# Optimization experiments

Measured on AMD Instinct MI355X. Metric: run time of the kernel, lower is better.

## Reference

```python
import jax, jax.numpy as jnp
import numpy as np

U, I, D = 100000, 200000, 64   # users, items, emb_size
N = U + I                      # total nodes
NNZ = 6400000                  # adjacency non-zeros
B = 4096                       # batch of (user,item) pairs
L = 3                          # n_layers


def setup_inputs() -> dict:
    key = jax.random.key(0)
    ks = jax.random.split(key, 11)
    s = 1.0 / np.sqrt(D)  # xavier-ish scale
    return {
        "user_emb_online": jax.random.normal(ks[0], (U, D), jnp.float32) * s,
        "item_emb_online": jax.random.normal(ks[1], (I, D), jnp.float32) * s,
        "user_emb_target": jax.random.normal(ks[2], (U, D), jnp.float32) * s,
        "item_emb_target": jax.random.normal(ks[3], (I, D), jnp.float32) * s,
        # normalized adjacency values (positive, roughly 1/deg scale)
        "adj_val": jax.random.uniform(ks[4], (NNZ,), jnp.float32) * (1.0 / 16.0),
        "pred_w": jax.random.normal(ks[5], (D, D), jnp.float32) * s,
        "pred_b": jnp.zeros((D,), jnp.float32),
        "adj_row": jax.random.randint(ks[6], (NNZ,), 0, N, dtype=jnp.int32),
        "adj_col": jax.random.randint(ks[7], (NNZ,), 0, N, dtype=jnp.int32),
        "user_idx": jax.random.randint(ks[8], (B,), 0, U, dtype=jnp.int32),
        "item_idx": jax.random.randint(ks[9], (B,), 0, I, dtype=jnp.int32),
    }


def _spmm(row, col, val, x):
    # sparse [N,N] @ dense [N,D] via gather + segment-sum
    return jax.ops.segment_sum(val[:, None] * x[col], row, num_segments=N)


def _lgcn_encode(user_emb, item_emb, row, col, val):
    ego = jnp.concatenate([user_emb, item_emb], axis=0)  # [N, D]
    acc = ego
    x = ego
    for _ in range(L):
        x = _spmm(row, col, val, x)
        acc = acc + x
    all_emb = acc / (L + 1)  # mean over stacked layer outputs
    return all_emb[:U], all_emb[U:]


def reference(user_emb_online, item_emb_online, user_emb_target, item_emb_target,
              adj_val, pred_w, pred_b, adj_row, adj_col, user_idx, item_idx):
    u_on_all, i_on_all = _lgcn_encode(user_emb_online, item_emb_online, adj_row, adj_col, adj_val)
    u_tg_all, i_tg_all = _lgcn_encode(user_emb_target, item_emb_target, adj_row, adj_col, adj_val)
    u_online = u_on_all[user_idx]   # [B, D]
    i_online = i_on_all[item_idx]
    u_target = u_tg_all[user_idx]
    i_target = i_tg_all[item_idx]
    u_pred = u_online @ pred_w.T + pred_b  # nn.Linear
    i_pred = i_online @ pred_w.T + pred_b
    return (u_pred, u_target, i_pred, i_target)
```

## Files before the change

kernel.cpp:

```cpp
#include <hip/hip_runtime.h>
#include <hip/hip_bf16.h>
#include <stdint.h>

#define U_N   100000
#define I_N   200000
#define NN    300000
#define DD    64
#define NNZ_N 6400000
#define BB    4096
#define CHUNK 4096
#define NB    ((NN + CHUNK - 1) / CHUNK)
#define NBK   74
#define EPB   4096
#define NSB   1184
#define SUBCAP 6656
#define BKCAP  94208
#define BKBLK  23
#define LBLK   48000

typedef unsigned short u16;
typedef unsigned int   u32;
typedef float vf2 __attribute__((ext_vector_type(2)));

__device__ __forceinline__ u16 f2bf(float f) {
    u32 u = __float_as_uint(f);
    u32 r = (u + 0x7FFFu + ((u >> 16) & 1u)) >> 16;
    return (u16)r;
}


#if __has_builtin(__builtin_amdgcn_cvt_pk_f32_fp8) && __has_builtin(__builtin_amdgcn_cvt_pk_fp8_f32)
#define FP8_HW 1
#else
#define FP8_HW 0
#endif

__device__ __forceinline__ u32 enc1_fp8(float f) {
    float af = fabsf(f);
    u32 s = (__float_as_uint(f) >> 31) << 7;
    if (af >= 0.015625f) {
        u32 au = __float_as_uint(af);
        u32 r = au + 0x7FFFFu + ((au >> 20) & 1u);
        u32 e = (r >> 23) - 120u;
        u32 m = (r >> 20) & 7u;
        if (e > 15u) { e = 15u; m = 6u; }
        return s | (e << 3) | m;
    } else {
        u32 q = (u32)__float2int_rn(af * 512.0f);
        return s | q;
    }
}

__device__ __forceinline__ u32 pack4_fp8(float a, float b, float c, float d) {
#if FP8_HW
    u32 w = 0;
    w = (u32)__builtin_amdgcn_cvt_pk_fp8_f32(a, b, (int)w, false);
    w = (u32)__builtin_amdgcn_cvt_pk_fp8_f32(c, d, (int)w, true);
    return w;
#else
    return enc1_fp8(a) | (enc1_fp8(b) << 8) | (enc1_fp8(c) << 16) | (enc1_fp8(d) << 24);
#endif
}

__device__ __forceinline__ float dec1_fp8(u32 b) {
    u32 s = (b & 0x80u) << 24;
    u32 e = (b >> 3) & 15u;
    u32 m = b & 7u;
    float mag = e ? __uint_as_float(((e + 120u) << 23) | (m << 20))
                  : (float)m * 0.001953125f;
    return __uint_as_float(__float_as_uint(mag) | s);
}

__device__ __forceinline__ void dec_fp8x4(u32 w, float* f) {
#if FP8_HW
    vf2 lo = __builtin_amdgcn_cvt_pk_f32_fp8((int)w, false);
    vf2 hi = __builtin_amdgcn_cvt_pk_f32_fp8((int)w, true);
    f[0] = lo[0]; f[1] = lo[1]; f[2] = hi[0]; f[3] = hi[1];
#else
    f[0] = dec1_fp8(w & 255u); f[1] = dec1_fp8((w >> 8) & 255u);
    f[2] = dec1_fp8((w >> 16) & 255u); f[3] = dec1_fp8(w >> 24);
#endif
}


__global__ void setup_k(unsigned char* __restrict__ mark, unsigned char* __restrict__ bmark,
                        int* __restrict__ nlist, int* __restrict__ bkt_cursor) {
    int tid = blockIdx.x * 256 + threadIdx.x;
    if (tid < NN / 4) { ((u32*)mark)[tid] = 0; ((u32*)bmark)[tid] = 0; }
    if (tid < NBK) bkt_cursor[tid] = tid * BKCAP;
    if (tid == NN / 4) nlist[0] = 0;
}


__global__ __launch_bounds__(256) void p1_k(const int* __restrict__ adj_row,
                                            const int* __restrict__ adj_col,
                                            const float* __restrict__ adj_val,
                                            int* __restrict__ bkt_cursor,
                                            u32* __restrict__ bpk,
                                            float* __restrict__ bval) {
    __shared__ int lcnt[NBK];
    __shared__ int lbase[NBK];
    int base = blockIdx.x * EPB;
    for (int i = threadIdx.x; i < NBK; i += 256) lcnt[i] = 0;
    __syncthreads();
    u32 pk[16]; float vv[16]; int bb[16]; int rk[16];
#pragma unroll
    for (int j = 0; j < 16; j++) {
        int e = base + j * 256 + threadIdx.x;
        bb[j] = -1;
        if (e < NNZ_N) {
            int r = adj_row[e];
            int c = adj_col[e];
            vv[j] = adj_val[e];
            int b = r >> 12;
            pk[j] = ((u32)(r & 4095) << 19) | (u32)c;
            bb[j] = b;
            rk[j] = atomicAdd(&lcnt[b], 1);
        }
    }
    __syncthreads();
    for (int i = threadIdx.x; i < NBK; i += 256)
        lbase[i] = atomicAdd(&bkt_cursor[i], lcnt[i]);
    __syncthreads();
#pragma unroll
    for (int j = 0; j < 16; j++) {
        if (bb[j] >= 0) {
            int p = lbase[bb[j]] + rk[j];
            bpk[p]  = pk[j];
            bval[p] = vv[j];
        }
    }
}


__global__ __launch_bounds__(1024) void bhist_k(const int* __restrict__ bkt_cursor,
                                                const u32* __restrict__ bpk,
                                                int* __restrict__ cnt) {
    __shared__ int h[4096];
    int b = blockIdx.x;
    int base = b * BKCAP;
    int e1 = bkt_cursor[b];
    for (int j = threadIdx.x; j < 4096; j += 1024) h[j] = 0;
    __syncthreads();
    for (int i = base + threadIdx.x; i < e1; i += 1024)
        atomicAdd(&h[bpk[i] >> 19], 1);
    __syncthreads();
    int rb = b << 12;
    for (int j = threadIdx.x; j < 4096; j += 1024) {
        int idx = rb + j;
        if (idx < NN) cnt[idx] = h[j];
    }
}


__global__ void scan1_k(const int* __restrict__ cnt, int* __restrict__ bsums) {
    __shared__ int red[256];
    int base = blockIdx.x * CHUNK;
    int s = 0;
    for (int j = threadIdx.x; j < CHUNK; j += 256) {
        int idx = base + j;
        s += (idx < NN) ? cnt[idx] : 0;
    }
    red[threadIdx.x] = s;
    __syncthreads();
    for (int o = 128; o > 0; o >>= 1) {
        if (threadIdx.x < o) red[threadIdx.x] += red[threadIdx.x + o];
        __syncthreads();
    }
    if (threadIdx.x == 0) bsums[blockIdx.x] = red[0];
}

__global__ void scan2_k(int* __restrict__ bsums, int* __restrict__ row_ptr) {
    __shared__ int sh[128];
    int v = (threadIdx.x < NB) ? bsums[threadIdx.x] : 0;
    sh[threadIdx.x] = v;
    __syncthreads();
    for (int o = 1; o < 128; o <<= 1) {
        int t = (threadIdx.x >= o) ? sh[threadIdx.x - o] : 0;
        __syncthreads();
        sh[threadIdx.x] += t;
        __syncthreads();
    }
    if (threadIdx.x < NB) bsums[threadIdx.x] = sh[threadIdx.x] - v;
    if (threadIdx.x == 127) row_ptr[NN] = sh[127];
}

__global__ void scan3_k(const int* __restrict__ cnt, const int* __restrict__ bsums,
                        int* __restrict__ row_ptr, int* __restrict__ sub_cursor) {
    __shared__ int tsum[256];
    int base = blockIdx.x * CHUNK;
    int loc[16];
    int s = 0;
#pragma unroll
    for (int j = 0; j < 16; j++) {
        int idx = base + threadIdx.x * 16 + j;
        int c = (idx < NN) ? cnt[idx] : 0;
        loc[j] = s;
        s += c;
    }
    tsum[threadIdx.x] = s;
    __syncthreads();
    int v = s;
    for (int o = 1; o < 256; o <<= 1) {
        int t = (threadIdx.x >= o) ? tsum[threadIdx.x - o] : 0;
        __syncthreads();
        tsum[threadIdx.x] += t;
        __syncthreads();
    }
    int texcl = tsum[threadIdx.x] - v;
    int boff = bsums[blockIdx.x];
#pragma unroll
    for (int j = 0; j < 16; j++) {
        int idx = base + threadIdx.x * 16 + j;
        if (idx < NN) {
            int val = boff + texcl + loc[j];
            row_ptr[idx] = val;
            if ((idx & 255) == 0) sub_cursor[idx >> 8] = val;
        }
    }
}


__global__ __launch_bounds__(256) void p2r_k(const int* __restrict__ bkt_cursor,
                                             const u32* __restrict__ bpk,
                                             const float* __restrict__ bval,
                                             int* __restrict__ sub_cursor,
                                             int2* __restrict__ mid) {
    __shared__ int lcnt[16], lbase[16], sbase[16];
    __shared__ int2 stage[4096];
    int b = blockIdx.y;
    int e1 = bkt_cursor[b];
    int base = b * BKCAP + blockIdx.x * 4096;
    if (base >= e1) return;
    if (threadIdx.x < 16) lcnt[threadIdx.x] = 0;
    __syncthreads();
    u32 pk[16]; float vv[16]; int sb[16], rk[16];
#pragma unroll
    for (int j = 0; j < 16; j++) {
        int e = base + j * 256 + threadIdx.x;
        sb[j] = -1;
        if (e < e1) {
            pk[j] = bpk[e];
            vv[j] = bval[e];
            int s = (int)((pk[j] >> 27) & 15u);
            sb[j] = s;
            rk[j] = atomicAdd(&lcnt[s], 1);
        }
    }
    __syncthreads();
    if (threadIdx.x == 0) {
        int acc = 0;
#pragma unroll
        for (int s = 0; s < 16; s++) { sbase[s] = acc; acc += lcnt[s]; }
    }
    if (threadIdx.x < 16)
        lbase[threadIdx.x] = atomicAdd(&sub_cursor[b * 16 + threadIdx.x], lcnt[threadIdx.x]);
    __syncthreads();
#pragma unroll
    for (int j = 0; j < 16; j++)
        if (sb[j] >= 0)
            stage[sbase[sb[j]] + rk[j]] = make_int2((int)pk[j], __float_as_int(vv[j]));
    __syncthreads();
    for (int s = 0; s < 16; s++) {
        int c = lcnt[s], gb = lbase[s], lb = sbase[s];
        for (int i = threadIdx.x; i < c; i += 256)
            mid[gb + i] = stage[lb + i];
    }
}


__global__ __launch_bounds__(256) void p3_k(const int* __restrict__ row_ptr,
                                            const int2* __restrict__ mid,
                                            int2* __restrict__ edge_s) {
    __shared__ int rbase[256], rcur[256];
    __shared__ int2 stage[SUBCAP];
    int s = blockIdx.x;
    int r0 = s << 8;
    if (r0 >= NN) return;
    int r1 = min(r0 + 256, NN);
    int nr = r1 - r0;
    int ebase = row_ptr[r0];
    int eend  = row_ptr[r1];
    int cnt = eend - ebase;
    if (threadIdx.x < nr) {
        rbase[threadIdx.x] = row_ptr[r0 + threadIdx.x] - ebase;
        rcur[threadIdx.x] = 0;
    }
    __syncthreads();
    for (int i = threadIdx.x; i < cnt; i += 256) {
        int2 d = mid[ebase + i];
        u32 pk = (u32)d.x;
        int l = (int)((pk >> 19) & 255u);
        int pos = rbase[l] + atomicAdd(&rcur[l], 1);
        if (pos < SUBCAP) stage[pos] = make_int2((int)(pk & 0x7FFFFu), d.y);
    }
    __syncthreads();
    for (int i = threadIdx.x; i < cnt; i += 256) edge_s[ebase + i] = stage[i];
}


__global__ void mark_k(const int* __restrict__ row_ptr, const int2* __restrict__ edge_s,
                       const int* __restrict__ user_idx, const int* __restrict__ item_idx,
                       unsigned char* __restrict__ mark, unsigned char* __restrict__ bmark) {
    int wave = threadIdx.x >> 6;
    int lane = threadIdx.x & 63;
    int slot = blockIdx.x * 4 + wave;
    if (slot >= 2 * BB) return;
    int r = (slot < BB) ? user_idx[slot] : U_N + item_idx[slot - BB];
    if (lane == 0) { mark[r] = 1; bmark[r] = 1; }
    int e0 = row_ptr[r], e1 = row_ptr[r + 1];
    for (int e = e0 + lane; e < e1; e += 64) mark[edge_s[e].x] = 1;
}

__global__ void compact_k(const unsigned char* __restrict__ mark,
                          int* __restrict__ list2, int* __restrict__ nlist) {
    int i = blockIdx.x * 256 + threadIdx.x;
    int lane = threadIdx.x & 63;
    int m = (i < NN) ? (int)mark[i] : 0;
    unsigned long long b = __ballot(m != 0);
    int pre = __popcll(b & ((1ull << lane) - 1ull));
    int tot = __popcll(b);
    int base = 0;
    if (lane == 0 && tot) base = atomicAdd(nlist, tot);
    base = __shfl(base, 0);
    if (m) list2[base + pre] = i;
}


__global__ void pack1_k(const float* __restrict__ ue_on, const float* __restrict__ ie_on,
                        const float* __restrict__ ue_tg, const float* __restrict__ ie_tg,
                        unsigned char* __restrict__ x0f) {
    int tid = blockIdx.x * blockDim.x + threadIdx.x;
    int n = tid >> 4;
    int t = tid & 15;
    if (n >= NN) return;
    const float* src;
    int soff;
    if (t < 8) {
        soff = t * 8;
        src = (n < U_N) ? ue_on + (size_t)n * 64 : ie_on + (size_t)(n - U_N) * 64;
    } else {
        soff = (t - 8) * 8;
        src = (n < U_N) ? ue_tg + (size_t)n * 64 : ie_tg + (size_t)(n - U_N) * 64;
    }
    float4 f0 = *(const float4*)(src + soff);
    float4 f1 = *(const float4*)(src + soff + 4);
    uint2 o;
    o.x = pack4_fp8(f0.x, f0.y, f0.z, f0.w);
    o.y = pack4_fp8(f1.x, f1.y, f1.z, f1.w);
    *(uint2*)(x0f + (size_t)n * 128 + t * 8) = o;
}


struct acc8 { float a[8]; };

__device__ __forceinline__ void red8(acc8& A) {
#pragma unroll
    for (int k = 0; k < 8; k++) {
        A.a[k] += __shfl_xor(A.a[k], 16);
        A.a[k] += __shfl_xor(A.a[k], 32);
    }
}

__device__ __forceinline__ void rg8_core(const int2* __restrict__ edge_s,
                                         const unsigned char* __restrict__ xf,
                                         int t, int g, int e0, int e1, acc8& A) {
#pragma unroll
    for (int k = 0; k < 8; k++) A.a[k] = 0.f;
    const unsigned char* xt = xf + t * 8;
    int d = e1 - e0;

    int2 ed[8];
    uint2 pv[8];
#pragma unroll
    for (int q = 0; q < 8; q++) { ed[q] = make_int2(0, 0); pv[q] = make_uint2(0u, 0u); }
#pragma unroll
    for (int q = 0; q < 8; q++) {
        int j = g + 4 * q;
        if (j < d) ed[q] = edge_s[e0 + j];
    }
#pragma unroll
    for (int q = 0; q < 8; q++) {
        int j = g + 4 * q;
        if (j < d) pv[q] = *(const uint2*)(xt + (size_t)((u32)ed[q].x * 128u));
    }
#pragma unroll
    for (int q = 0; q < 8; q++) {
        float v = __int_as_float(ed[q].y);
        float f[8];
        dec_fp8x4(pv[q].x, f);
        dec_fp8x4(pv[q].y, f + 4);
#pragma unroll
        for (int k = 0; k < 8; k++) A.a[k] += v * f[k];
    }
    for (int e = e0 + 32 + g * 4; e < e1; e += 16) {
        int m = e1 - e;
#pragma unroll
        for (int k = 0; k < 4; k++) {
            if (k < m) {
                int2 dd = edge_s[e + k];
                float v = __int_as_float(dd.y);
                uint2 p = *(const uint2*)(xt + (size_t)((u32)dd.x * 128u));
                float f[8];
                dec_fp8x4(p.x, f);
                dec_fp8x4(p.y, f + 4);
#pragma unroll
                for (int q = 0; q < 8; q++) A.a[q] += v * f[q];
            }
        }
    }
    red8(A);
}

__global__ __launch_bounds__(256) void spmm1_k(const int* __restrict__ row_ptr,
                                               const int2* __restrict__ edge_s,
                                               const unsigned char* __restrict__ x0f,
                                               const unsigned char* __restrict__ bmark,
                                               u16* __restrict__ y,
                                               unsigned char* __restrict__ yf) {
    int lane = threadIdx.x & 63;
    int t = lane & 15, g = lane >> 4;
    int r = blockIdx.x * 4 + (threadIdx.x >> 6);
    if (r >= NN) return;
    acc8 A;
    rg8_core(edge_s, x0f, t, g, row_ptr[r], row_ptr[r + 1], A);
    if (g == 0) {
        uint2 of;
        of.x = pack4_fp8(A.a[0], A.a[1], A.a[2], A.a[3]);
        of.y = pack4_fp8(A.a[4], A.a[5], A.a[6], A.a[7]);
        *(uint2*)(yf + (size_t)r * 128 + t * 8) = of;
        if (bmark[r]) {
            uint4 o;
            o.x = ((u32)f2bf(A.a[1]) << 16) | (u32)f2bf(A.a[0]);
            o.y = ((u32)f2bf(A.a[3]) << 16) | (u32)f2bf(A.a[2]);
            o.z = ((u32)f2bf(A.a[5]) << 16) | (u32)f2bf(A.a[4]);
            o.w = ((u32)f2bf(A.a[7]) << 16) | (u32)f2bf(A.a[6]);
            *(uint4*)(y + (size_t)r * 128 + t * 8) = o;
        }
    }
}

__device__ __forceinline__ void rg16_core(const int2* __restrict__ edge_s,
                                          const u16* __restrict__ x,
                                          int t, int g, int e0, int e1, acc8& A) {
#pragma unroll
    for (int k = 0; k < 8; k++) A.a[k] = 0.f;
    const u16* xt = x + t * 8;
    int d = e1 - e0;

    int2 ed[8];
    uint4 pv[8];
#pragma unroll
    for (int q = 0; q < 8; q++) { ed[q] = make_int2(0, 0); pv[q] = make_uint4(0u, 0u, 0u, 0u); }
#pragma unroll
    for (int q = 0; q < 8; q++) {
        int j = g + 4 * q;
        if (j < d) ed[q] = edge_s[e0 + j];
    }
#pragma unroll
    for (int q = 0; q < 8; q++) {
        int j = g + 4 * q;
        if (j < d) pv[q] = *(const uint4*)(xt + (size_t)(u32)ed[q].x * 128);
    }
#pragma unroll
    for (int q = 0; q < 8; q++) {
        float v = __int_as_float(ed[q].y);
        A.a[0] += v * __uint_as_float(pv[q].x << 16);
        A.a[1] += v * __uint_as_float(pv[q].x & 0xFFFF0000u);
        A.a[2] += v * __uint_as_float(pv[q].y << 16);
        A.a[3] += v * __uint_as_float(pv[q].y & 0xFFFF0000u);
        A.a[4] += v * __uint_as_float(pv[q].z << 16);
        A.a[5] += v * __uint_as_float(pv[q].z & 0xFFFF0000u);
        A.a[6] += v * __uint_as_float(pv[q].w << 16);
        A.a[7] += v * __uint_as_float(pv[q].w & 0xFFFF0000u);
    }
    for (int e = e0 + 32 + g * 4; e < e1; e += 16) {
        int m = e1 - e;
#pragma unroll
        for (int k = 0; k < 4; k++) {
            if (k < m) {
                int2 dd = edge_s[e + k];
                float v = __int_as_float(dd.y);
                uint4 p = *(const uint4*)(xt + (size_t)(u32)dd.x * 128);
                A.a[0] += v * __uint_as_float(p.x << 16);
                A.a[1] += v * __uint_as_float(p.x & 0xFFFF0000u);
                A.a[2] += v * __uint_as_float(p.y << 16);
                A.a[3] += v * __uint_as_float(p.y & 0xFFFF0000u);
                A.a[4] += v * __uint_as_float(p.z << 16);
                A.a[5] += v * __uint_as_float(p.z & 0xFFFF0000u);
                A.a[6] += v * __uint_as_float(p.w << 16);
                A.a[7] += v * __uint_as_float(p.w & 0xFFFF0000u);
            }
        }
    }
    red8(A);
}

__global__ __launch_bounds__(256) void spmm_list_k(const int* __restrict__ row_ptr,
                                                   const int2* __restrict__ edge_s,
                                                   const unsigned char* __restrict__ x1f,
                                                   u16* __restrict__ y,
                                                   const int* __restrict__ list2,
                                                   const int* __restrict__ nlist) {
    int lane = threadIdx.x & 63;
    int t = lane & 15, g = lane >> 4;
    int slot = blockIdx.x * 4 + (threadIdx.x >> 6);
    if (slot >= *nlist) return;
    int r = list2[slot];
    acc8 A;
    rg8_core(edge_s, x1f, t, g, row_ptr[r], row_ptr[r + 1], A);
    if (g == 0) {
        uint4 o;
        o.x = ((u32)f2bf(A.a[1]) << 16) | (u32)f2bf(A.a[0]);
        o.y = ((u32)f2bf(A.a[3]) << 16) | (u32)f2bf(A.a[2]);
        o.z = ((u32)f2bf(A.a[5]) << 16) | (u32)f2bf(A.a[4]);
        o.w = ((u32)f2bf(A.a[7]) << 16) | (u32)f2bf(A.a[6]);
        *(uint4*)(y + (size_t)r * 128 + t * 8) = o;
    }
}

__global__ __launch_bounds__(256) void spmm_last_k(const int* __restrict__ row_ptr,
                                                   const int2* __restrict__ edge_s,
                                                   const u16* __restrict__ x,
                                                   const int* __restrict__ user_idx,
                                                   const int* __restrict__ item_idx,
                                                   float* __restrict__ out_acc) {
    int lane = threadIdx.x & 63;
    int t = lane & 15, g = lane >> 4;
    int slot = blockIdx.x * 4 + (threadIdx.x >> 6);
    if (slot >= 2 * BB) return;
    int r = (slot < BB) ? user_idx[slot] : U_N + item_idx[slot - BB];
    acc8 A;
    rg16_core(edge_s, x, t, g, row_ptr[r], row_ptr[r + 1], A);
    if (g == 0) {
        uint4 p = *(const uint4*)(x + (size_t)r * 128 + t * 8);
        A.a[0] += __uint_as_float(p.x << 16);
        A.a[1] += __uint_as_float(p.x & 0xFFFF0000u);
        A.a[2] += __uint_as_float(p.y << 16);
        A.a[3] += __uint_as_float(p.y & 0xFFFF0000u);
        A.a[4] += __uint_as_float(p.z << 16);
        A.a[5] += __uint_as_float(p.z & 0xFFFF0000u);
        A.a[6] += __uint_as_float(p.w << 16);
        A.a[7] += __uint_as_float(p.w & 0xFFFF0000u);
        float4* p0 = (float4*)(out_acc + (size_t)slot * 128 + t * 8);
        float4 c0 = p0[0], c1 = p0[1];
        c0.x += A.a[0]; c0.y += A.a[1]; c0.z += A.a[2]; c0.w += A.a[3];
        c1.x += A.a[4]; c1.y += A.a[5]; c1.z += A.a[6]; c1.w += A.a[7];
        p0[0] = c0; p0[1] = c1;
    }
}


__global__ void init_acc_k(const int* __restrict__ user_idx, const int* __restrict__ item_idx,
                           const float* __restrict__ ue_on, const float* __restrict__ ie_on,
                           const float* __restrict__ ue_tg, const float* __restrict__ ie_tg,
                           float* __restrict__ out_acc) {
    int t = blockIdx.x * blockDim.x + threadIdx.x;
    int slot = t >> 5;
    int j = t & 31;
    if (slot >= 2 * BB) return;
    int node = (slot < BB) ? user_idx[slot] : U_N + item_idx[slot - BB];
    const float* src;
    int soff, doff;
    if (j < 16) {
        soff = j * 4; doff = j * 4;
        src = (node < U_N) ? ue_on + (size_t)node * 64 : ie_on + (size_t)(node - U_N) * 64;
    } else {
        soff = (j - 16) * 4; doff = 64 + (j - 16) * 4;
        src = (node < U_N) ? ue_tg + (size_t)node * 64 : ie_tg + (size_t)(node - U_N) * 64;
    }
    float4 f = *(const float4*)(src + soff);
    *(float4*)(out_acc + (size_t)slot * 128 + doff) = f;
}

__global__ void gadd_k(const int* __restrict__ user_idx, const int* __restrict__ item_idx,
                       const u16* __restrict__ x, float* __restrict__ out_acc) {
    int t = blockIdx.x * blockDim.x + threadIdx.x;
    int slot = t >> 6;
    int l = t & 63;
    if (slot >= 2 * BB) return;
    int node = (slot < BB) ? user_idx[slot] : U_N + item_idx[slot - BB];
    u32 p = *(const u32*)(x + (size_t)node * 128 + (l << 1));
    float fx = __uint_as_float(p << 16);
    float fy = __uint_as_float(p & 0xFFFF0000u);
    float2* q = (float2*)(out_acc + (size_t)slot * 128) + l;
    float2 cur = *q;
    cur.x += fx; cur.y += fy;
    *q = cur;
}


__global__ __launch_bounds__(256) void pred_k(const float* __restrict__ out_acc,
                                              const float* __restrict__ W,
                                              const float* __restrict__ bias,
                                              float* __restrict__ out) {
    __shared__ float wld[64 * 65];
    __shared__ float uld[4 * 64];
    int j = threadIdx.x & 63;
    int rl = threadIdx.x >> 6;
    for (int i = threadIdx.x; i < 4096; i += 256) {
        int jj = i >> 6, kk = i & 63;
        wld[kk * 65 + jj] = W[i];
    }
    int slot = blockIdx.x * 4 + rl;
    uld[rl * 64 + j] = out_acc[(size_t)slot * 128 + j] * 0.25f;
    float tv = out_acc[(size_t)slot * 128 + 64 + j] * 0.25f;
    size_t tdst = (slot < BB) ? (size_t)BB * 64 + (size_t)slot * 64 + j
                              : (size_t)3 * BB * 64 + (size_t)(slot - BB) * 64 + j;
    out[tdst] = tv;
    __syncthreads();
    float acc = bias[j];
#pragma unroll
    for (int k = 0; k < 64; k++) acc += uld[rl * 64 + k] * wld[k * 65 + j];
    size_t dst = (slot < BB) ? (size_t)slot * 64 + j
                             : (size_t)2 * BB * 64 + (size_t)(slot - BB) * 64 + j;
    out[dst] = acc;
}


extern "C" void kernel_launch(void* const* d_in, const int* in_sizes, int n_in,
                              void* d_out, int out_size, void* d_ws, size_t ws_size,
                              hipStream_t stream) {
    const float* ue_on = (const float*)d_in[0];
    const float* ie_on = (const float*)d_in[1];
    const float* ue_tg = (const float*)d_in[2];
    const float* ie_tg = (const float*)d_in[3];
    const float* adj_val = (const float*)d_in[4];
    const float* pred_w = (const float*)d_in[5];
    const float* pred_b = (const float*)d_in[6];
    const int* adj_row = (const int*)d_in[7];
    const int* adj_col = (const int*)d_in[8];
    const int* user_idx = (const int*)d_in[9];
    const int* item_idx = (const int*)d_in[10];
    float* out = (float*)d_out;

    char* ws = (char*)d_ws;
    size_t off = 0;
    auto alloc = [&](size_t bytes) -> char* {
        char* p = ws + off;
        off = (off + bytes + 255) & ~(size_t)255;
        return p;
    };
    int*   cnt        = (int*)alloc((size_t)NN * 4);
    int*   row_ptr    = (int*)alloc((size_t)(NN + 1) * 4);
    int*   bsums      = (int*)alloc(256 * 4);
    int*   bkt_cursor = (int*)alloc(256 * 4);
    int*   sub_cursor = (int*)alloc((size_t)NSB * 4);
    unsigned char* mark = (unsigned char*)alloc((size_t)NN);
    unsigned char* bmark = (unsigned char*)alloc((size_t)NN);
    int*   list2      = (int*)alloc((size_t)NN * 4);
    int*   nlist      = (int*)alloc(256 * 4);
    int2*  edge_s     = (int2*)alloc((size_t)NNZ_N * 8);
    u16*   x_a        = (u16*)alloc((size_t)NN * 128 * 2);
    u16*   x_b        = (u16*)alloc((size_t)NN * 128 * 2);
    float* out_acc    = (float*)alloc((size_t)2 * BB * 128 * 4);

    u32*   bpk  = (u32*)x_a;
    unsigned char* x0f = (unsigned char*)x_a;
    unsigned char* x1f = (unsigned char*)x_a + (size_t)NN * 128;
    float* bval = (float*)x_b;
    int2*  mid  = edge_s;

    (void)n_in; (void)in_sizes; (void)out_size; (void)ws_size;

    setup_k<<<294, 256, 0, stream>>>(mark, bmark, nlist, bkt_cursor);
    p1_k<<<(NNZ_N + EPB - 1) / EPB, 256, 0, stream>>>(adj_row, adj_col, adj_val, bkt_cursor, bpk, bval);
    bhist_k<<<NBK, 1024, 0, stream>>>(bkt_cursor, bpk, cnt);
    scan1_k<<<NB, 256, 0, stream>>>(cnt, bsums);
    scan2_k<<<1, 128, 0, stream>>>(bsums, row_ptr);
    scan3_k<<<NB, 256, 0, stream>>>(cnt, bsums, row_ptr, sub_cursor);
    p2r_k<<<dim3(BKBLK, NBK), 256, 0, stream>>>(bkt_cursor, bpk, bval, sub_cursor, mid);
    p3_k<<<NSB, 256, 0, stream>>>(row_ptr, mid, edge_s);

    mark_k<<<(2 * BB) / 4, 256, 0, stream>>>(row_ptr, edge_s, user_idx, item_idx, mark, bmark);
    compact_k<<<(NN + 255) / 256, 256, 0, stream>>>(mark, list2, nlist);

    pack1_k<<<(NN * 16 + 255) / 256, 256, 0, stream>>>(ue_on, ie_on, ue_tg, ie_tg, x0f);
    init_acc_k<<<(2 * BB * 32) / 256, 256, 0, stream>>>(user_idx, item_idx, ue_on, ie_on, ue_tg, ie_tg, out_acc);

    spmm1_k<<<NN / 4, 256, 0, stream>>>(row_ptr, edge_s, x0f, bmark, x_b, x1f);
    gadd_k<<<(2 * BB * 64) / 256, 256, 0, stream>>>(user_idx, item_idx, x_b, out_acc);
    spmm_list_k<<<LBLK, 256, 0, stream>>>(row_ptr, edge_s, x1f, x_b, list2, nlist);
    spmm_last_k<<<(2 * BB) / 4, 256, 0, stream>>>(row_ptr, edge_s, x_b, user_idx, item_idx, out_acc);

    pred_k<<<(2 * BB) / 4, 256, 0, stream>>>(out_acc, pred_w, pred_b, out);
}
```

Before: 748.0 us.

## Fuse bucketing, fp8 packing and acc init; derive scan sums from bucket counts

Merges the edge bucketing pass, the fp8 packing of input embeddings and the batch accumulator init into one launch using block-index ranges. It also folds the bucket histogram and the block-sum scan into a single kernel, taking per-chunk sums straight from bucket cursors, since bucket size equals chunk size. The bucketed keys move to the upper half of x_b so packing into x_a does not clash. This cuts launch overhead and lets independent work overlap, at the cost of more register pressure in the combined kernels.

```diff
diff --git a/kernel.cpp b/kernel.cpp
--- a/kernel.cpp
+++ b/kernel.cpp
@@ -17,6 +17,9 @@
 #define BKCAP  94208
 #define BKBLK  23
 #define LBLK   48000
+#define P1B   ((NNZ_N + EPB - 1) / EPB)
+#define PACKB ((NN * 16) / 256)
+#define ACCB  ((2 * BB * 32) / 256)
 
 typedef unsigned short u16;
 typedef unsigned int   u32;
@@ -92,97 +95,140 @@
 }
 
 
-__global__ __launch_bounds__(256) void p1_k(const int* __restrict__ adj_row,
-                                            const int* __restrict__ adj_col,
-                                            const float* __restrict__ adj_val,
-                                            int* __restrict__ bkt_cursor,
-                                            u32* __restrict__ bpk,
-                                            float* __restrict__ bval) {
+__global__ __launch_bounds__(256) void fused1_k(const int* __restrict__ adj_row,
+                                                const int* __restrict__ adj_col,
+                                                const float* __restrict__ adj_val,
+                                                int* __restrict__ bkt_cursor,
+                                                u32* __restrict__ bpk,
+                                                float* __restrict__ bval,
+                                                const float* __restrict__ ue_on,
+                                                const float* __restrict__ ie_on,
+                                                const float* __restrict__ ue_tg,
+                                                const float* __restrict__ ie_tg,
+                                                unsigned char* __restrict__ x0f,
+                                                const int* __restrict__ user_idx,
+                                                const int* __restrict__ item_idx,
+                                                float* __restrict__ out_acc) {
     __shared__ int lcnt[NBK];
     __shared__ int lbase[NBK];
-    int base = blockIdx.x * EPB;
-    for (int i = threadIdx.x; i < NBK; i += 256) lcnt[i] = 0;
-    __syncthreads();
-    u32 pk[16]; float vv[16]; int bb[16]; int rk[16];
-#pragma unroll
-    for (int j = 0; j < 16; j++) {
-        int e = base + j * 256 + threadIdx.x;
-        bb[j] = -1;
-        if (e < NNZ_N) {
-            int r = adj_row[e];
-            int c = adj_col[e];
-            vv[j] = adj_val[e];
-            int b = r >> 12;
-            pk[j] = ((u32)(r & 4095) << 19) | (u32)c;
-            bb[j] = b;
-            rk[j] = atomicAdd(&lcnt[b], 1);
-        }
-    }
-    __syncthreads();
-    for (int i = threadIdx.x; i < NBK; i += 256)
-        lbase[i] = atomicAdd(&bkt_cursor[i], lcnt[i]);
-    __syncthreads();
-#pragma unroll
-    for (int j = 0; j < 16; j++) {
-        if (bb[j] >= 0) {
-            int p = lbase[bb[j]] + rk[j];
-            bpk[p]  = pk[j];
-            bval[p] = vv[j];
-        }
-    }
-}
-
-
-__global__ __launch_bounds__(1024) void bhist_k(const int* __restrict__ bkt_cursor,
-                                                const u32* __restrict__ bpk,
-                                                int* __restrict__ cnt) {
-    __shared__ int h[4096];
-    int b = blockIdx.x;
-    int base = b * BKCAP;
-    int e1 = bkt_cursor[b];
-    for (int j = threadIdx.x; j < 4096; j += 1024) h[j] = 0;
-    __syncthreads();
-    for (int i = base + threadIdx.x; i < e1; i += 1024)
-        atomicAdd(&h[bpk[i] >> 19], 1);
-    __syncthreads();
-    int rb = b << 12;
-    for (int j = threadIdx.x; j < 4096; j += 1024) {
-        int idx = rb + j;
-        if (idx < NN) cnt[idx] = h[j];
-    }
-}
-
-
-__global__ void scan1_k(const int* __restrict__ cnt, int* __restrict__ bsums) {
-    __shared__ int red[256];
-    int base = blockIdx.x * CHUNK;
-    int s = 0;
-    for (int j = threadIdx.x; j < CHUNK; j += 256) {
-        int idx = base + j;
-        s += (idx < NN) ? cnt[idx] : 0;
-    }
-    red[threadIdx.x] = s;
-    __syncthreads();
-    for (int o = 128; o > 0; o >>= 1) {
-        if (threadIdx.x < o) red[threadIdx.x] += red[threadIdx.x + o];
-        __syncthreads();
-    }
-    if (threadIdx.x == 0) bsums[blockIdx.x] = red[0];
-}
-
-__global__ void scan2_k(int* __restrict__ bsums, int* __restrict__ row_ptr) {
-    __shared__ int sh[128];
-    int v = (threadIdx.x < NB) ? bsums[threadIdx.x] : 0;
-    sh[threadIdx.x] = v;
-    __syncthreads();
-    for (int o = 1; o < 128; o <<= 1) {
-        int t = (threadIdx.x >= o) ? sh[threadIdx.x - o] : 0;
-        __syncthreads();
-        sh[threadIdx.x] += t;
-        __syncthreads();
-    }
-    if (threadIdx.x < NB) bsums[threadIdx.x] = sh[threadIdx.x] - v;
-    if (threadIdx.x == 127) row_ptr[NN] = sh[127];
+    int bid = blockIdx.x;
+    if (bid < P1B) {
+        int base = bid * EPB;
+        for (int i = threadIdx.x; i < NBK; i += 256) lcnt[i] = 0;
+        __syncthreads();
+        u32 pk[16]; float vv[16]; int bb[16]; int rk[16];
+#pragma unroll
+        for (int j = 0; j < 16; j++) {
+            int e = base + j * 256 + threadIdx.x;
+            bb[j] = -1;
+            if (e < NNZ_N) {
+                int r = adj_row[e];
+                int c = adj_col[e];
+                vv[j] = adj_val[e];
+                int b = r >> 12;
+                pk[j] = ((u32)(r & 4095) << 19) | (u32)c;
+                bb[j] = b;
+                rk[j] = atomicAdd(&lcnt[b], 1);
+            }
+        }
+        __syncthreads();
+        for (int i = threadIdx.x; i < NBK; i += 256)
+            lbase[i] = atomicAdd(&bkt_cursor[i], lcnt[i]);
+        __syncthreads();
+#pragma unroll
+        for (int j = 0; j < 16; j++) {
+            if (bb[j] >= 0) {
+                int p = lbase[bb[j]] + rk[j];
+                bpk[p]  = pk[j];
+                bval[p] = vv[j];
+            }
+        }
+        return;
+    }
+    bid -= P1B;
+    if (bid < PACKB) {
+        int tid = bid * 256 + threadIdx.x;
+        int n = tid >> 4;
+        int t = tid & 15;
+        if (n >= NN) return;
+        const float* src;
+        int soff;
+        if (t < 8) {
+            soff = t * 8;
+            src = (n < U_N) ? ue_on + (size_t)n * 64 : ie_on + (size_t)(n - U_N) * 64;
+        } else {
+            soff = (t - 8) * 8;
+            src = (n < U_N) ? ue_tg + (size_t)n * 64 : ie_tg + (size_t)(n - U_N) * 64;
+        }
+        float4 f0 = *(const float4*)(src + soff);
+        float4 f1 = *(const float4*)(src + soff + 4);
+        uint2 o;
+        o.x = pack4_fp8(f0.x, f0.y, f0.z, f0.w);
+        o.y = pack4_fp8(f1.x, f1.y, f1.z, f1.w);
+        *(uint2*)(x0f + (size_t)n * 128 + t * 8) = o;
+        return;
+    }
+    bid -= PACKB;
+    {
+        int t = bid * 256 + threadIdx.x;
+        int slot = t >> 5;
+        int j = t & 31;
+        if (slot >= 2 * BB) return;
+        int node = (slot < BB) ? user_idx[slot] : U_N + item_idx[slot - BB];
+        const float* src;
+        int soff, doff;
+        if (j < 16) {
+            soff = j * 4; doff = j * 4;
+            src = (node < U_N) ? ue_on + (size_t)node * 64 : ie_on + (size_t)(node - U_N) * 64;
+        } else {
+            soff = (j - 16) * 4; doff = 64 + (j - 16) * 4;
+            src = (node < U_N) ? ue_tg + (size_t)node * 64 : ie_tg + (size_t)(node - U_N) * 64;
+        }
+        float4 f = *(const float4*)(src + soff);
+        *(float4*)(out_acc + (size_t)slot * 128 + doff) = f;
+    }
+}
+
+
+__global__ __launch_bounds__(1024) void fused2_k(const int* __restrict__ bkt_cursor,
+                                                 const u32* __restrict__ bpk,
+                                                 int* __restrict__ cnt,
+                                                 int* __restrict__ bsums,
+                                                 int* __restrict__ row_ptr) {
+    if (blockIdx.x < NBK) {
+        __shared__ int h[4096];
+        int b = blockIdx.x;
+        int base = b * BKCAP;
+        int e1 = bkt_cursor[b];
+        for (int j = threadIdx.x; j < 4096; j += 1024) h[j] = 0;
+        __syncthreads();
+        for (int i = base + threadIdx.x; i < e1; i += 1024)
+            atomicAdd(&h[bpk[i] >> 19], 1);
+        __syncthreads();
+        int rb = b << 12;
+        for (int j = threadIdx.x; j < 4096; j += 1024) {
+            int idx = rb + j;
+            if (idx < NN) cnt[idx] = h[j];
+        }
+    } else {
+        __shared__ int sh[128];
+        int t = threadIdx.x;
+        int v = 0;
+        if (t < 128) {
+            v = (t < NB) ? bkt_cursor[t] - t * BKCAP : 0;
+            sh[t] = v;
+        }
+        __syncthreads();
+        for (int o = 1; o < 128; o <<= 1) {
+            int tmp = 0;
+            if (t < 128 && t >= o) tmp = sh[t - o];
+            __syncthreads();
+            if (t < 128) sh[t] += tmp;
+            __syncthreads();
+        }
+        if (t < NB) bsums[t] = sh[t] - v;
+        if (t == 127) row_ptr[NN] = sh[127];
+    }
 }
 
 __global__ void scan3_k(const int* __restrict__ cnt, const int* __restrict__ bsums,
@@ -324,31 +370,6 @@
     if (lane == 0 && tot) base = atomicAdd(nlist, tot);
     base = __shfl(base, 0);
     if (m) list2[base + pre] = i;
-}
-
-
-__global__ void pack1_k(const float* __restrict__ ue_on, const float* __restrict__ ie_on,
-                        const float* __restrict__ ue_tg, const float* __restrict__ ie_tg,
-                        unsigned char* __restrict__ x0f) {
-    int tid = blockIdx.x * blockDim.x + threadIdx.x;
-    int n = tid >> 4;
-    int t = tid & 15;
-    if (n >= NN) return;
-    const float* src;
-    int soff;
-    if (t < 8) {
-        soff = t * 8;
-        src = (n < U_N) ? ue_on + (size_t)n * 64 : ie_on + (size_t)(n - U_N) * 64;
-    } else {
-        soff = (t - 8) * 8;
-        src = (n < U_N) ? ue_tg + (size_t)n * 64 : ie_tg + (size_t)(n - U_N) * 64;
-    }
-    float4 f0 = *(const float4*)(src + soff);
-    float4 f1 = *(const float4*)(src + soff + 4);
-    uint2 o;
-    o.x = pack4_fp8(f0.x, f0.y, f0.z, f0.w);
-    o.y = pack4_fp8(f1.x, f1.y, f1.z, f1.w);
-    *(uint2*)(x0f + (size_t)n * 128 + t * 8) = o;
 }
 
 
@@ -551,28 +572,6 @@
 }
 
 
-__global__ void init_acc_k(const int* __restrict__ user_idx, const int* __restrict__ item_idx,
-                           const float* __restrict__ ue_on, const float* __restrict__ ie_on,
-                           const float* __restrict__ ue_tg, const float* __restrict__ ie_tg,
-                           float* __restrict__ out_acc) {
-    int t = blockIdx.x * blockDim.x + threadIdx.x;
-    int slot = t >> 5;
-    int j = t & 31;
-    if (slot >= 2 * BB) return;
-    int node = (slot < BB) ? user_idx[slot] : U_N + item_idx[slot - BB];
-    const float* src;
-    int soff, doff;
-    if (j < 16) {
-        soff = j * 4; doff = j * 4;
-        src = (node < U_N) ? ue_on + (size_t)node * 64 : ie_on + (size_t)(node - U_N) * 64;
-    } else {
-        soff = (j - 16) * 4; doff = 64 + (j - 16) * 4;
-        src = (node < U_N) ? ue_tg + (size_t)node * 64 : ie_tg + (size_t)(node - U_N) * 64;
-    }
-    float4 f = *(const float4*)(src + soff);
-    *(float4*)(out_acc + (size_t)slot * 128 + doff) = f;
-}
-
 __global__ void gadd_k(const int* __restrict__ user_idx, const int* __restrict__ item_idx,
                        const u16* __restrict__ x, float* __restrict__ out_acc) {
     int t = blockIdx.x * blockDim.x + threadIdx.x;
@@ -655,28 +654,26 @@
     u16*   x_b        = (u16*)alloc((size_t)NN * 128 * 2);
     float* out_acc    = (float*)alloc((size_t)2 * BB * 128 * 4);
 
-    u32*   bpk  = (u32*)x_a;
     unsigned char* x0f = (unsigned char*)x_a;
     unsigned char* x1f = (unsigned char*)x_a + (size_t)NN * 128;
     float* bval = (float*)x_b;
+    u32*   bpk  = (u32*)((char*)x_b + (size_t)NN * 128);
     int2*  mid  = edge_s;
 
     (void)n_in; (void)in_sizes; (void)out_size; (void)ws_size;
 
     setup_k<<<294, 256, 0, stream>>>(mark, bmark, nlist, bkt_cursor);
-    p1_k<<<(NNZ_N + EPB - 1) / EPB, 256, 0, stream>>>(adj_row, adj_col, adj_val, bkt_cursor, bpk, bval);
-    bhist_k<<<NBK, 1024, 0, stream>>>(bkt_cursor, bpk, cnt);
-    scan1_k<<<NB, 256, 0, stream>>>(cnt, bsums);
-    scan2_k<<<1, 128, 0, stream>>>(bsums, row_ptr);
+    fused1_k<<<P1B + PACKB + ACCB, 256, 0, stream>>>(adj_row, adj_col, adj_val,
+                                                     bkt_cursor, bpk, bval,
+                                                     ue_on, ie_on, ue_tg, ie_tg, x0f,
+                                                     user_idx, item_idx, out_acc);
+    fused2_k<<<NBK + 1, 1024, 0, stream>>>(bkt_cursor, bpk, cnt, bsums, row_ptr);
     scan3_k<<<NB, 256, 0, stream>>>(cnt, bsums, row_ptr, sub_cursor);
     p2r_k<<<dim3(BKBLK, NBK), 256, 0, stream>>>(bkt_cursor, bpk, bval, sub_cursor, mid);
     p3_k<<<NSB, 256, 0, stream>>>(row_ptr, mid, edge_s);
 
     mark_k<<<(2 * BB) / 4, 256, 0, stream>>>(row_ptr, edge_s, user_idx, item_idx, mark, bmark);
     compact_k<<<(NN + 255) / 256, 256, 0, stream>>>(mark, list2, nlist);
-
-    pack1_k<<<(NN * 16 + 255) / 256, 256, 0, stream>>>(ue_on, ie_on, ue_tg, ie_tg, x0f);
-    init_acc_k<<<(2 * BB * 32) / 256, 256, 0, stream>>>(user_idx, item_idx, ue_on, ie_on, ue_tg, ie_tg, out_acc);
 
     spmm1_k<<<NN / 4, 256, 0, stream>>>(row_ptr, edge_s, x0f, bmark, x_b, x1f);
     gadd_k<<<(2 * BB * 64) / 256, 256, 0, stream>>>(user_idx, item_idx, x_b, out_acc);
```

Measured after the change: 738.4 us. About the same (-1.3%).
